# Performance work log

Hardware: AMD Instinct MI355X
Metric: run time of the kernel (lower is better)

## Reference

```python
import jax, jax.numpy as jnp
import numpy as np

B = 2; N_RAW = 16384; N_KP = 2048; M_VOX = 8192; C_VOX = 64
H_BEV, W_BEV, C_BEV, BEV_STRIDE = 200, 176, 256, 8
VOXEL_SIZE = np.array([0.05, 0.05, 0.1], np.float32)
PC_MIN = np.array([0.0, -40.0, -3.0], np.float32)
DOWNSAMPLE = 4
RAW_RADII = (0.4, 0.8); RAW_NS = (16, 16)
CONV_RADII = (1.2, 2.4); CONV_NS = (16, 32)
BN_SCALE = float(1.0 / np.sqrt(1.0 + 1e-5))  # eval-mode BN, running mean=0 var=1


def _fps_idx(pts, n):
    # farthest point sampling over pts [N,3] -> [n] int32 indices
    N = pts.shape[0]
    def step(carry, _):
        dists, last = carry
        d = jnp.sum((pts - pts[last]) ** 2, axis=-1)
        dists = jnp.minimum(dists, d)
        nxt = jnp.argmax(dists).astype(jnp.int32)
        return (dists, nxt), nxt
    init = (jnp.full((N,), 1e10, pts.dtype), jnp.int32(0))
    _, rest = jax.lax.scan(step, init, None, length=n - 1)
    return jnp.concatenate([jnp.zeros((1,), jnp.int32), rest])


def _bilinear(bev, x, y):
    # bev [H,W,C]; faithful to bilinear_interpolate_bev (clamp then weight)
    H, W, _ = bev.shape
    xf = jnp.floor(x); yf = jnp.floor(y)
    x0 = jnp.clip(xf.astype(jnp.int32), 0, W - 1)
    x1 = jnp.clip(xf.astype(jnp.int32) + 1, 0, W - 1)
    y0 = jnp.clip(yf.astype(jnp.int32), 0, H - 1)
    y1 = jnp.clip(yf.astype(jnp.int32) + 1, 0, H - 1)
    fa = bev[y1, x0]; fb = bev[y1, x1]; fc = bev[y0, x1]; fd = bev[y0, x0]
    x0f = x0.astype(x.dtype); x1f = x1.astype(x.dtype)
    y0f = y0.astype(y.dtype); y1f = y1.astype(y.dtype)
    wa = (x - x0f) * (y1f - y); wb = (x1f - x) * (y1f - y)
    wc = (x1f - x) * (y - y0f); wd = (x - x0f) * (y - y0f)
    return fd * wb[:, None] + fc * wa[:, None] + fa * wc[:, None] + fb * wd[:, None]


def _group(xyz, feats, new_xyz, radius, nsample):
    # ball query: first nsample points within radius (original order), pad with first hit
    M = xyz.shape[0]
    d2 = jnp.sum((new_xyz[:, None, :] - xyz[None, :, :]) ** 2, axis=-1)  # [K,M]
    mask = d2 < radius * radius
    key = jnp.where(mask, jnp.arange(M, dtype=jnp.int32)[None, :], M)
    idx = jnp.sort(key, axis=1)[:, :nsample]
    empty = ~jnp.any(mask, axis=1)
    idx = jnp.where(idx < M, idx, idx[:, :1])
    idx = jnp.clip(idx, 0, M - 1)
    g_xyz = xyz[idx] - new_xyz[:, None, :]
    g = jnp.concatenate([g_xyz, feats[idx]], axis=-1)  # [K,ns,3+C]
    return jnp.where(empty[:, None, None], 0.0, g), empty


def _bn_relu(x, g, b):
    return jax.nn.relu(x * (g * BN_SCALE) + b)


def _sa(xyz, feats, new_xyz, radii, nss, w0, g0, b0, w1, g1, b1):
    outs = []
    for i, (r, ns) in enumerate(zip(radii, nss)):
        grouped, empty = jax.vmap(lambda x, f, nx: _group(x, f, nx, r, ns))(xyz, feats, new_xyz)
        h = _bn_relu(grouped @ w0[i], g0[i], b0[i])
        h = _bn_relu(h @ w1[i], g1[i], b1[i])
        pooled = jnp.max(h, axis=2)  # [B,K,Cout]
        outs.append(jnp.where(empty[..., None], 0.0, pooled))
    return jnp.concatenate(outs, axis=-1)


def _forward(points, spatial_features, voxel_coords, voxel_features,
             raw_w0, raw_g0, raw_b0, raw_w1, raw_g1, raw_b1,
             conv_w0, conv_g0, conv_b0, conv_w1, conv_g1, conv_b1,
             fusion_w, fusion_g, fusion_b):
    pts = points.reshape(B, N_RAW, -1)
    xyz_raw = pts[..., 1:4]
    idxs = jax.vmap(lambda p: _fps_idx(p, N_KP))(jax.lax.stop_gradient(xyz_raw))
    kp = jnp.take_along_axis(xyz_raw, idxs[..., None], axis=1)  # [B,NKP,3]
    xi = (kp[..., 0] - PC_MIN[0]) / VOXEL_SIZE[0] / BEV_STRIDE
    yi = (kp[..., 1] - PC_MIN[1]) / VOXEL_SIZE[1] / BEV_STRIDE
    bev = jnp.transpose(spatial_features, (0, 2, 3, 1))  # [B,H,W,C]
    bev_feat = jax.vmap(_bilinear)(bev, xi, yi)  # [B,NKP,C_BEV]
    raw_feat = _sa(xyz_raw, pts[..., 4:], kp, RAW_RADII, RAW_NS,
                   raw_w0, raw_g0, raw_b0, raw_w1, raw_g1, raw_b1)
    vc = voxel_coords.reshape(B, M_VOX, 4)
    centers = (vc[..., jnp.array([3, 2, 1])].astype(jnp.float32) + 0.5) \
        * jnp.asarray(VOXEL_SIZE * DOWNSAMPLE) + jnp.asarray(PC_MIN)
    conv_feat = _sa(centers, voxel_features.reshape(B, M_VOX, C_VOX), kp, CONV_RADII, CONV_NS,
                    conv_w0, conv_g0, conv_b0, conv_w1, conv_g1, conv_b1)
    feats = jnp.concatenate([bev_feat, raw_feat, conv_feat], axis=-1).reshape(B * N_KP, -1)
    return _bn_relu(feats @ fusion_w, fusion_g, fusion_b)  # [B*NKP, 128]


def setup_inputs():
    key = jax.random.key(0)
    ks = jax.random.split(key, 8)
    xyz = jax.random.uniform(ks[0], (B * N_RAW, 3), jnp.float32) * jnp.array([70.4, 80.0, 4.0]) + jnp.array([0.0, -40.0, -3.0])
    inten = jax.random.uniform(ks[1], (B * N_RAW, 1), jnp.float32)
    bidx = jnp.repeat(jnp.arange(B, dtype=jnp.float32), N_RAW)[:, None]
    points = jnp.concatenate([bidx, xyz, inten], axis=1)
    spatial_features = jax.random.normal(ks[2], (B, C_BEV, H_BEV, W_BEV), jnp.float32)
    vb = jnp.repeat(jnp.arange(B, dtype=jnp.int32), M_VOX)[:, None]
    vz = jax.random.randint(ks[3], (B * M_VOX, 1), 0, 10, jnp.int32)
    vy = jax.random.randint(ks[4], (B * M_VOX, 1), 0, 400, jnp.int32)
    vx = jax.random.randint(ks[5], (B * M_VOX, 1), 0, 352, jnp.int32)
    voxel_coords = jnp.concatenate([vb, vz, vy, vx], axis=1)
    voxel_features = jax.random.normal(ks[6], (B * M_VOX, C_VOX), jnp.float32)
    pk = jax.random.split(ks[7], 5)
    w = lambda k, s: jax.random.normal(k, s, jnp.float32) * 0.05
    return dict(
        points=points, spatial_features=spatial_features,
        voxel_coords=voxel_coords, voxel_features=voxel_features,
        raw_w0=w(pk[0], (2, 4, 16)), raw_g0=jnp.ones((2, 16)), raw_b0=jnp.zeros((2, 16)),
        raw_w1=w(pk[1], (2, 16, 16)), raw_g1=jnp.ones((2, 16)), raw_b1=jnp.zeros((2, 16)),
        conv_w0=w(pk[2], (2, 67, 64)), conv_g0=jnp.ones((2, 64)), conv_b0=jnp.zeros((2, 64)),
        conv_w1=w(pk[3], (2, 64, 64)), conv_g1=jnp.ones((2, 64)), conv_b1=jnp.zeros((2, 64)),
        fusion_w=w(pk[4], (416, 128)), fusion_g=jnp.ones((128,)), fusion_b=jnp.zeros((128,)))


def reference(points, spatial_features, voxel_coords, voxel_features,
              raw_w0, raw_g0, raw_b0, raw_w1, raw_g1, raw_b1,
              conv_w0, conv_g0, conv_b0, conv_w1, conv_g1, conv_b1,
              fusion_w, fusion_g, fusion_b):
    return _forward(points, spatial_features, voxel_coords, voxel_features,
                    raw_w0, raw_g0, raw_b0, raw_w1, raw_g1, raw_b1,
                    conv_w0, conv_g0, conv_b0, conv_w1, conv_g1, conv_b1,
                    fusion_w, fusion_g, fusion_b)
```

## Files before the change

### kernel.cpp

```cpp
#include <hip/hip_runtime.h>


#define NRAW   16384
#define MVOX   8192
#define NKP    2048
#define NKPALL 4096

__device__ __constant__ float kBNS = (float)0.9999950000374997;

typedef float f32x2 __attribute__((ext_vector_type(2)));

__global__ __launch_bounds__(256) void prep_kernel(
    const float* __restrict__ pts, const int* __restrict__ vc,
    float4* __restrict__ xyz4, float4* __restrict__ cxyz4) {
#pragma clang fp contract(off)
  int i = blockIdx.x * 256 + threadIdx.x;
  if (i < 2 * NRAW) {
    const float* p = pts + (size_t)i * 5;
    xyz4[i] = make_float4(p[1], p[2], p[3], p[4]);
  }
  if (i < 2 * MVOX) {
    const int* v = vc + (size_t)i * 4;
    cxyz4[i] = make_float4(((float)v[3] + 0.5f) * 0.2f + 0.0f,
                           ((float)v[2] + 0.5f) * 0.2f + -40.0f,
                           ((float)v[1] + 0.5f) * 0.4f + -3.0f, 0.f);
  }
}

__global__ __launch_bounds__(1024) void sort_kernel(
    const float* __restrict__ pts, int* __restrict__ sperm) {
  const int b = blockIdx.x, t = threadIdx.x;
  __shared__ unsigned hist[256], cur[256];
  if (t < 256) hist[t] = 0u;
  __syncthreads();
  int bins[16];
#pragma unroll
  for (int k = 0; k < 16; ++k) {
    const int i = k * 1024 + t;
    const float y = pts[(size_t)(b * NRAW + i) * 5 + 2];
    int bin = (int)((y + 40.0f) * 3.2f);
    bin = bin < 0 ? 0 : (bin > 255 ? 255 : bin);
    bins[k] = bin;
    atomicAdd(&hist[bin], 1u);
  }
  __syncthreads();
  if (t == 0) {
    unsigned acc = 0;
    for (int i = 0; i < 256; ++i) { cur[i] = acc; acc += hist[i]; }
  }
  __syncthreads();
#pragma unroll
  for (int k = 0; k < 16; ++k) {
    const int i = k * 1024 + t;
    const unsigned pos = atomicAdd(&cur[bins[k]], 1u);
    sperm[b * NRAW + pos] = i;
  }
}

#define U64_STAGE(CTRL, RMASK)                                                 \
  {                                                                            \
    const unsigned tlo = (unsigned)__builtin_amdgcn_update_dpp(                \
        0, (int)lo, CTRL, RMASK, 0xf, true);                                   \
    const unsigned thi = (unsigned)__builtin_amdgcn_update_dpp(                \
        0, (int)hi, CTRL, RMASK, 0xf, true);                                   \
    const unsigned long long tv = ((unsigned long long)thi << 32) | tlo;       \
    const unsigned long long cv = ((unsigned long long)hi << 32) | lo;         \
    if (tv > cv) { hi = thi; lo = tlo; }                                       \
  }

__global__ __launch_bounds__(1024, 4) void fps_kernel(
    const int* __restrict__ sperm, const float4* __restrict__ xyz4,
    float* __restrict__ kx, float* __restrict__ ky, float* __restrict__ kz) {
#pragma clang fp contract(off)
  const int b = blockIdx.x;
  const int t = threadIdx.x;
  const int w = t >> 6, lane = t & 63;
  const int wb = w * 1024;
  const int base = b * NRAW;

  __shared__ unsigned long long slot[3];

  int pj[16];
  f32x2 px2[8], py2[8], pz2[8], dd2[8];
#pragma unroll
  for (int j = 0; j < 16; ++j)
    pj[j] = sperm[base + wb + j * 64 + lane];
#pragma unroll
  for (int j = 0; j < 16; ++j) {
    const float4 q = xyz4[base + pj[j]];
    px2[j >> 1][j & 1] = q.x;
    py2[j >> 1][j & 1] = q.y;
    pz2[j >> 1][j & 1] = q.z;
    dd2[j >> 1][j & 1] = 1e10f;
  }
  if (t < 3) slot[t] = 0ULL;

  float bnx = px2[0].x, bxx = px2[0].x, bny = py2[0].x, bxy = py2[0].x,
        bnz = pz2[0].x, bxz = pz2[0].x;
#pragma unroll
  for (int j = 1; j < 16; ++j) {
    bnx = fminf(bnx, px2[j >> 1][j & 1]); bxx = fmaxf(bxx, px2[j >> 1][j & 1]);
    bny = fminf(bny, py2[j >> 1][j & 1]); bxy = fmaxf(bxy, py2[j >> 1][j & 1]);
    bnz = fminf(bnz, pz2[j >> 1][j & 1]); bxz = fmaxf(bxz, pz2[j >> 1][j & 1]);
  }
#pragma unroll
  for (int off = 1; off < 64; off <<= 1) {
    bnx = fminf(bnx, __shfl_xor(bnx, off, 64));
    bxx = fmaxf(bxx, __shfl_xor(bxx, off, 64));
    bny = fminf(bny, __shfl_xor(bny, off, 64));
    bxy = fmaxf(bxy, __shfl_xor(bxy, off, 64));
    bnz = fminf(bnz, __shfl_xor(bnz, off, 64));
    bxz = fmaxf(bxz, __shfl_xor(bxz, off, 64));
  }

  const float4 p0 = xyz4[base];
  float lx = p0.x, ly = p0.y, lz = p0.z;
  if (t == 0) { kx[b * NKP] = lx; ky[b * NKP] = ly; kz[b * NKP] = lz; }

  unsigned long long cpk = 0ULL;
  float bvc = __builtin_inff();
  __syncthreads();

  for (int s = 1; s < NKP; ++s) {
    float dxm = fmaxf(fmaxf(bnx - lx, lx - bxx), 0.f);
    float dym = fmaxf(fmaxf(bny - ly, ly - bxy), 0.f);
    float dzm = fmaxf(fmaxf(bnz - lz, lz - bxz), 0.f);
    const float LB2 = dxm * dxm + dym * dym + dzm * dzm;
    if (!(LB2 * 0.9999f > bvc)) {
      const f32x2 lx2 = {lx, lx}, ly2 = {ly, ly}, lz2 = {lz, lz};
#pragma unroll
      for (int j8 = 0; j8 < 8; ++j8) {
        f32x2 dx = px2[j8] - lx2;
        f32x2 dy = py2[j8] - ly2;
        f32x2 dz = pz2[j8] - lz2;
        f32x2 d2 = dx * dx;
        d2 = d2 + dy * dy;
        d2 = d2 + dz * dz;
        dd2[j8] = __builtin_elementwise_min(dd2[j8], d2);
      }
      f32x2 t0 = __builtin_elementwise_max(dd2[0], dd2[1]);
      f32x2 t1 = __builtin_elementwise_max(dd2[2], dd2[3]);
      f32x2 t2 = __builtin_elementwise_max(dd2[4], dd2[5]);
      f32x2 t3 = __builtin_elementwise_max(dd2[6], dd2[7]);
      t0 = __builtin_elementwise_max(t0, t1);
      t2 = __builtin_elementwise_max(t2, t3);
      t0 = __builtin_elementwise_max(t0, t2);
      const float bv = fmaxf(t0.x, t0.y);
      const unsigned vb = __float_as_uint(bv);
      unsigned mo = 0xFFFFFFFFu;
#pragma unroll
      for (int j = 0; j < 16; ++j)
        if (__float_as_uint(dd2[j >> 1][j & 1]) == vb) {
          const unsigned o = (unsigned)pj[j];
          mo = o < mo ? o : mo;
        }
      unsigned hi = vb, lo = ~mo;
      U64_STAGE(0xB1,  0xf)
      U64_STAGE(0x4E,  0xf)
      U64_STAGE(0x124, 0xf)
      U64_STAGE(0x128, 0xf)
      U64_STAGE(0x142, 0xa)
      U64_STAGE(0x143, 0xc)
      bvc = __uint_as_float(
          (unsigned)__builtin_amdgcn_readlane((int)hi, 63));
      cpk = ((unsigned long long)hi << 32) | (unsigned long long)lo;
    }
    if (lane == 63) atomicMax(&slot[s % 3], cpk);
    __syncthreads();

    const unsigned long long g = slot[s % 3];
    const int wi = __builtin_amdgcn_readfirstlane((int)~(unsigned)g);
    if (t == 0) slot[(s + 2) % 3] = 0ULL;
    const float4 cw = xyz4[base + wi];
    lx = cw.x; ly = cw.y; lz = cw.z;
    if (t == 0) { kx[b * NKP + s] = lx; ky[b * NKP + s] = ly; kz[b * NKP + s] = lz; }
  }
}

__global__ __launch_bounds__(256) void bev_kernel(
    const float* __restrict__ sf, const float* __restrict__ kx,
    const float* __restrict__ ky, float* __restrict__ feats) {
#pragma clang fp contract(off)
  const int kidx = blockIdx.x;
  const int c = threadIdx.x;
  const int b = kidx >> 11;
  const float x = (kx[kidx] - 0.0f) / 0.05f / 8.0f;
  const float y = (ky[kidx] - (-40.0f)) / 0.05f / 8.0f;
  const float xf = floorf(x), yf = floorf(y);
  int x0 = (int)xf;     x0 = x0 < 0 ? 0 : (x0 > 175 ? 175 : x0);
  int x1 = (int)xf + 1; x1 = x1 < 0 ? 0 : (x1 > 175 ? 175 : x1);
  int y0 = (int)yf;     y0 = y0 < 0 ? 0 : (y0 > 199 ? 199 : y0);
  int y1 = (int)yf + 1; y1 = y1 < 0 ? 0 : (y1 > 199 ? 199 : y1);
  const float x0f = (float)x0, x1f = (float)x1, y0f = (float)y0, y1f = (float)y1;
  const float wa = (x - x0f) * (y1f - y);
  const float wb = (x1f - x) * (y1f - y);
  const float wc = (x1f - x) * (y - y0f);
  const float wd = (x - x0f) * (y - y0f);
  const float* base = sf + ((size_t)b * 256 + c) * (200 * 176);
  const float fa = base[y1 * 176 + x0];
  const float fb = base[y1 * 176 + x1];
  const float fc = base[y0 * 176 + x1];
  const float fd = base[y0 * 176 + x0];
  float r = fd * wb; r = r + fc * wa; r = r + fa * wc; r = r + fb * wd;
  feats[(size_t)kidx * 416 + c] = r;
}

__global__ __launch_bounds__(256) void raw_sa_kernel(
    const float4* __restrict__ xyz4,
    const float* __restrict__ kx, const float* __restrict__ ky,
    const float* __restrict__ kz,
    const float* __restrict__ w0, const float* __restrict__ g0,
    const float* __restrict__ b0, const float* __restrict__ w1,
    const float* __restrict__ g1, const float* __restrict__ b1,
    float* __restrict__ feats) {
  const int wv = threadIdx.x >> 6;
  const int lane = threadIdx.x & 63;
  const int gw = blockIdx.x * 4 + wv;
  const int ri = gw >> 12;
  const int kidx = gw & 4095;
  const int b = kidx >> 11;
  const float R2 = ri ? (float)(0.8 * 0.8) : (float)(0.4 * 0.4);

  __shared__ int   idxl[4][16];
  __shared__ float hbuf[4][16][17];

  const float kxv = kx[kidx], kyv = ky[kidx], kzv = kz[kidx];
  const int base = b * NRAW;
  int cnt = 0;
  {
#pragma clang fp contract(off)
    for (int ch = 0; ch < NRAW / 64 && cnt < 16; ++ch) {
      const float4 q = xyz4[base + ch * 64 + lane];
      float dx = kxv - q.x, dy = kyv - q.y, dz = kzv - q.z;
      float d2 = dx * dx; d2 = d2 + dy * dy; d2 = d2 + dz * dz;
      unsigned long long m = __ballot(d2 < R2);
      while (m && cnt < 16) {
        int bit = __builtin_ctzll(m);
        if (lane == 0) idxl[wv][cnt] = ch * 64 + bit;
        ++cnt;
        m &= m - 1;
      }
    }
  }
  const int outoff = kidx * 416 + 256 + ri * 16;
  if (cnt == 0) {
    if (lane < 16) feats[outoff + lane] = 0.f;
    return;
  }
  __threadfence_block();

  const int s = lane & 15, cq = lane >> 4;
  const int ss = (s < cnt) ? s : 0;
  const float4 q = xyz4[base + idxl[wv][ss]];
  const float gx = q.x - kxv, gy = q.y - kyv, gz = q.z - kzv, gi = q.w;
  const int wb0 = ri * 64, cb = ri * 16;
#pragma unroll
  for (int j = 0; j < 4; ++j) {
    int c = cq * 4 + j;
    float a = gx * w0[wb0 + c];
    a = fmaf(gy, w0[wb0 + 16 + c], a);
    a = fmaf(gz, w0[wb0 + 32 + c], a);
    a = fmaf(gi, w0[wb0 + 48 + c], a);
    a = fmaf(a, g0[cb + c] * kBNS, b0[cb + c]);
    hbuf[wv][s][c] = fmaxf(a, 0.f);
  }
  __threadfence_block();
  float o0 = 0.f, o1 = 0.f, o2 = 0.f, o3 = 0.f;
  const int wb1 = ri * 256;
#pragma unroll
  for (int k = 0; k < 16; ++k) {
    float hk = hbuf[wv][s][k];
    o0 = fmaf(hk, w1[wb1 + k * 16 + cq * 4 + 0], o0);
    o1 = fmaf(hk, w1[wb1 + k * 16 + cq * 4 + 1], o1);
    o2 = fmaf(hk, w1[wb1 + k * 16 + cq * 4 + 2], o2);
    o3 = fmaf(hk, w1[wb1 + k * 16 + cq * 4 + 3], o3);
  }
  float v0 = fmaxf(fmaf(o0, g1[cb + cq * 4 + 0] * kBNS, b1[cb + cq * 4 + 0]), 0.f);
  float v1 = fmaxf(fmaf(o1, g1[cb + cq * 4 + 1] * kBNS, b1[cb + cq * 4 + 1]), 0.f);
  float v2 = fmaxf(fmaf(o2, g1[cb + cq * 4 + 2] * kBNS, b1[cb + cq * 4 + 2]), 0.f);
  float v3 = fmaxf(fmaf(o3, g1[cb + cq * 4 + 3] * kBNS, b1[cb + cq * 4 + 3]), 0.f);
#pragma unroll
  for (int off = 1; off < 16; off <<= 1) {
    v0 = fmaxf(v0, __shfl_xor(v0, off, 64));
    v1 = fmaxf(v1, __shfl_xor(v1, off, 64));
    v2 = fmaxf(v2, __shfl_xor(v2, off, 64));
    v3 = fmaxf(v3, __shfl_xor(v3, off, 64));
  }
  if (s == 0) {
    feats[outoff + cq * 4 + 0] = v0;
    feats[outoff + cq * 4 + 1] = v1;
    feats[outoff + cq * 4 + 2] = v2;
    feats[outoff + cq * 4 + 3] = v3;
  }
}

__global__ __launch_bounds__(256) void conv_sa_kernel(
    const float4* __restrict__ cxyz4, const float* __restrict__ vf,
    const float* __restrict__ kx, const float* __restrict__ ky,
    const float* __restrict__ kz,
    const float* __restrict__ w0, const float* __restrict__ g0,
    const float* __restrict__ b0, const float* __restrict__ w1,
    const float* __restrict__ g1, const float* __restrict__ b1,
    float* __restrict__ feats) {
  const int wv = threadIdx.x >> 6;
  const int lane = threadIdx.x & 63;
  const int gw = blockIdx.x * 4 + wv;
  const int ri = gw >> 12;
  const int kidx = gw & 4095;
  const int b = kidx >> 11;
  const int NS = ri ? 32 : 16;
  const float R2 = ri ? (float)(2.4 * 2.4) : (float)(1.2 * 1.2);

  __shared__ int   idxl[4][32];
  __shared__ float gbuf[4][64];
  __shared__ float hbuf[4][32][64];

  const float kxv = kx[kidx], kyv = ky[kidx], kzv = kz[kidx];
  const int base = b * MVOX;
  int cnt = 0;
  {
#pragma clang fp contract(off)
    for (int ch = 0; ch < MVOX / 64 && cnt < NS; ++ch) {
      const float4 q = cxyz4[base + ch * 64 + lane];
      float dx = kxv - q.x, dy = kyv - q.y, dz = kzv - q.z;
      float d2 = dx * dx; d2 = d2 + dy * dy; d2 = d2 + dz * dz;
      unsigned long long m = __ballot(d2 < R2);
      while (m && cnt < NS) {
        int bit = __builtin_ctzll(m);
        if (lane == 0) idxl[wv][cnt] = ch * 64 + bit;
        ++cnt;
        m &= m - 1;
      }
    }
  }
  const int outoff = kidx * 416 + 288 + ri * 64;
  if (cnt == 0) {
    feats[outoff + lane] = 0.f;
    return;
  }
  __threadfence_block();

  const float wA0 = w0[(ri * 67 + 0) * 64 + lane];
  const float wA1 = w0[(ri * 67 + 1) * 64 + lane];
  const float wA2 = w0[(ri * 67 + 2) * 64 + lane];
  float wB[64];
#pragma unroll
  for (int k = 0; k < 64; ++k) wB[k] = w0[(ri * 67 + 3 + k) * 64 + lane];
  float wC[64];
#pragma unroll
  for (int k = 0; k < 64; ++k) wC[k] = w1[(ri * 64 + k) * 64 + lane];
  const float s0 = g0[ri * 64 + lane] * kBNS, bb0 = b0[ri * 64 + lane];
  const float s1 = g1[ri * 64 + lane] * kBNS, bb1 = b1[ri * 64 + lane];

  for (int sm = 0; sm < cnt; ++sm) {
    const int p = base + idxl[wv][sm];
    const float4 q = cxyz4[p];
    const float ox = q.x - kxv, oy = q.y - kyv, oz = q.z - kzv;
    gbuf[wv][lane] = vf[(size_t)p * 64 + lane];
    __threadfence_block();
    float acc = ox * wA0;
    acc = fmaf(oy, wA1, acc);
    acc = fmaf(oz, wA2, acc);
#pragma unroll
    for (int k4 = 0; k4 < 16; ++k4) {
      float4 g4 = *(const float4*)&gbuf[wv][k4 * 4];
      acc = fmaf(g4.x, wB[k4 * 4 + 0], acc);
      acc = fmaf(g4.y, wB[k4 * 4 + 1], acc);
      acc = fmaf(g4.z, wB[k4 * 4 + 2], acc);
      acc = fmaf(g4.w, wB[k4 * 4 + 3], acc);
    }
    hbuf[wv][sm][lane] = fmaxf(fmaf(acc, s0, bb0), 0.f);
    __threadfence_block();
  }
  float mx = -1e30f;
  for (int sm = 0; sm < cnt; ++sm) {
    float acc = 0.f;
#pragma unroll
    for (int k4 = 0; k4 < 16; ++k4) {
      float4 h4 = *(const float4*)&hbuf[wv][sm][k4 * 4];
      acc = fmaf(h4.x, wC[k4 * 4 + 0], acc);
      acc = fmaf(h4.y, wC[k4 * 4 + 1], acc);
      acc = fmaf(h4.z, wC[k4 * 4 + 2], acc);
      acc = fmaf(h4.w, wC[k4 * 4 + 3], acc);
    }
    mx = fmaxf(mx, fmaxf(fmaf(acc, s1, bb1), 0.f));
  }
  feats[outoff + lane] = mx;
}

__global__ __launch_bounds__(256) void fusion_kernel(
    const float* __restrict__ feats, const float* __restrict__ fw,
    const float* __restrict__ fg, const float* __restrict__ fb,
    float* __restrict__ out) {
  const int gid = blockIdx.x * 256 + threadIdx.x;
  const int kidx = gid >> 7, c = gid & 127;
  const float* f = feats + (size_t)kidx * 416;
  float acc = 0.f;
#pragma unroll 4
  for (int k = 0; k < 416; k += 4) {
    float4 fv = *(const float4*)(f + k);
    acc = fmaf(fv.x, fw[(k + 0) * 128 + c], acc);
    acc = fmaf(fv.y, fw[(k + 1) * 128 + c], acc);
    acc = fmaf(fv.z, fw[(k + 2) * 128 + c], acc);
    acc = fmaf(fv.w, fw[(k + 3) * 128 + c], acc);
  }
  out[gid] = fmaxf(fmaf(acc, fg[c] * kBNS, fb[c]), 0.f);
}

extern "C" void kernel_launch(void* const* d_in, const int* in_sizes, int n_in,
                              void* d_out, int out_size, void* d_ws, size_t ws_size,
                              hipStream_t stream) {
  (void)in_sizes; (void)n_in; (void)out_size; (void)ws_size;
  const float* pts = (const float*)d_in[0];
  const float* sf  = (const float*)d_in[1];
  const int*   vc  = (const int*)d_in[2];
  const float* vf  = (const float*)d_in[3];
  const float* raw_w0 = (const float*)d_in[4];
  const float* raw_g0 = (const float*)d_in[5];
  const float* raw_b0 = (const float*)d_in[6];
  const float* raw_w1 = (const float*)d_in[7];
  const float* raw_g1 = (const float*)d_in[8];
  const float* raw_b1 = (const float*)d_in[9];
  const float* conv_w0 = (const float*)d_in[10];
  const float* conv_g0 = (const float*)d_in[11];
  const float* conv_b0 = (const float*)d_in[12];
  const float* conv_w1 = (const float*)d_in[13];
  const float* conv_g1 = (const float*)d_in[14];
  const float* conv_b1 = (const float*)d_in[15];
  const float* fus_w = (const float*)d_in[16];
  const float* fus_g = (const float*)d_in[17];
  const float* fus_b = (const float*)d_in[18];
  float* out = (float*)d_out;

  float* W = (float*)d_ws;
  float4* xyz4  = (float4*)W;
  float4* cxyz4 = (float4*)(W + 131072);
  float* kx    = W + 196608;
  float* ky    = W + 200704;
  float* kz    = W + 204800;
  float* feats = W + 208896;
  int* sperm = (int*)(W + 208896);

  prep_kernel<<<128, 256, 0, stream>>>(pts, vc, xyz4, cxyz4);
  sort_kernel<<<2, 1024, 0, stream>>>(pts, sperm);
  fps_kernel<<<2, 1024, 0, stream>>>(sperm, xyz4, kx, ky, kz);
  bev_kernel<<<NKPALL, 256, 0, stream>>>(sf, kx, ky, feats);
  raw_sa_kernel<<<2048, 256, 0, stream>>>(xyz4, kx, ky, kz,
                                          raw_w0, raw_g0, raw_b0, raw_w1, raw_g1, raw_b1,
                                          feats);
  conv_sa_kernel<<<2048, 256, 0, stream>>>(cxyz4, vf, kx, ky, kz,
                                           conv_w0, conv_g0, conv_b0, conv_w1, conv_g1, conv_b1,
                                           feats);
  fusion_kernel<<<2048, 256, 0, stream>>>(feats, fus_w, fus_g, fus_b, out);
}
```

Measured before the change: 2.198 ms.

## Fuse FPS with downstream stages via persistent workers polling progress flags

Merges the FPS, BEV sampling, raw and voxel set-abstraction and fusion kernels into one persistent launch. Two blocks run FPS and publish a release-ordered progress counter every 16 keypoints, while 224 worker blocks spin on that counter and process each keypoint as soon as it exists. Per-keypoint features stay in LDS instead of a global buffer, and conv weights are staged in LDS rather than per-lane registers. This hides the downstream work behind the serial FPS loop, at the cost of relying on all blocks being co-resident (risk of deadlock otherwise), spin-wait overhead, and workers competing with the FPS blocks for CU resources.

New measurement: 3.135 ms. 42.6% more time.

```diff
diff --git a/kernel.cpp b/kernel.cpp
--- a/kernel.cpp
+++ b/kernel.cpp
@@ -1,10 +1,12 @@
 #include <hip/hip_runtime.h>
 
 
-#define NRAW   16384
-#define MVOX   8192
-#define NKP    2048
-#define NKPALL 4096
+#define NRAW    16384
+#define MVOX    8192
+#define NKP     2048
+#define NKPALL  4096
+#define NWORKER 224
+#define NBLK    (NWORKER + 2)
 
 __device__ __constant__ float kBNS = (float)0.9999950000374997;
 
@@ -68,343 +70,337 @@
     if (tv > cv) { hi = thi; lo = tlo; }                                       \
   }
 
-__global__ __launch_bounds__(1024, 4) void fps_kernel(
+__global__ __launch_bounds__(1024, 1) void fused_kernel(
     const int* __restrict__ sperm, const float4* __restrict__ xyz4,
-    float* __restrict__ kx, float* __restrict__ ky, float* __restrict__ kz) {
+    const float4* __restrict__ cxyz4, const float* __restrict__ vf,
+    const float* __restrict__ sf,
+    const float* __restrict__ rw0, const float* __restrict__ rg0,
+    const float* __restrict__ rb0, const float* __restrict__ rw1,
+    const float* __restrict__ rg1, const float* __restrict__ rb1,
+    const float* __restrict__ cw0, const float* __restrict__ cg0,
+    const float* __restrict__ cb0, const float* __restrict__ cw1,
+    const float* __restrict__ cg1, const float* __restrict__ cb1,
+    const float* __restrict__ fw, const float* __restrict__ fg,
+    const float* __restrict__ fb,
+    float* __restrict__ kx, float* __restrict__ ky, float* __restrict__ kz,
+    int* prog, float* __restrict__ out) {
+  const int t = threadIdx.x;
+  const int wv = t >> 6, lane = t & 63;
+
+  __shared__ unsigned long long slot[3];
+  __shared__ float ldsW0[2 * 67 * 64];
+  __shared__ float ldsW1[2 * 64 * 64];
+  __shared__ int   idxlC[2][32];
+  __shared__ __align__(16) float gbuf[2][64];
+  __shared__ __align__(16) float hbufC[2][32][64];
+  __shared__ int   idxlR[2][16];
+  __shared__ float hbufR[2][16][17];
+  __shared__ __align__(16) float featsL[416];
+  __shared__ float kxyz[4];
+
+  if (blockIdx.x < 2) {
 #pragma clang fp contract(off)
-  const int b = blockIdx.x;
-  const int t = threadIdx.x;
-  const int w = t >> 6, lane = t & 63;
-  const int wb = w * 1024;
-  const int base = b * NRAW;
-
-  __shared__ unsigned long long slot[3];
-
-  int pj[16];
-  f32x2 px2[8], py2[8], pz2[8], dd2[8];
-#pragma unroll
-  for (int j = 0; j < 16; ++j)
-    pj[j] = sperm[base + wb + j * 64 + lane];
-#pragma unroll
-  for (int j = 0; j < 16; ++j) {
-    const float4 q = xyz4[base + pj[j]];
-    px2[j >> 1][j & 1] = q.x;
-    py2[j >> 1][j & 1] = q.y;
-    pz2[j >> 1][j & 1] = q.z;
-    dd2[j >> 1][j & 1] = 1e10f;
-  }
-  if (t < 3) slot[t] = 0ULL;
-
-  float bnx = px2[0].x, bxx = px2[0].x, bny = py2[0].x, bxy = py2[0].x,
-        bnz = pz2[0].x, bxz = pz2[0].x;
-#pragma unroll
-  for (int j = 1; j < 16; ++j) {
-    bnx = fminf(bnx, px2[j >> 1][j & 1]); bxx = fmaxf(bxx, px2[j >> 1][j & 1]);
-    bny = fminf(bny, py2[j >> 1][j & 1]); bxy = fmaxf(bxy, py2[j >> 1][j & 1]);
-    bnz = fminf(bnz, pz2[j >> 1][j & 1]); bxz = fmaxf(bxz, pz2[j >> 1][j & 1]);
-  }
-#pragma unroll
-  for (int off = 1; off < 64; off <<= 1) {
-    bnx = fminf(bnx, __shfl_xor(bnx, off, 64));
-    bxx = fmaxf(bxx, __shfl_xor(bxx, off, 64));
-    bny = fminf(bny, __shfl_xor(bny, off, 64));
-    bxy = fmaxf(bxy, __shfl_xor(bxy, off, 64));
-    bnz = fminf(bnz, __shfl_xor(bnz, off, 64));
-    bxz = fmaxf(bxz, __shfl_xor(bxz, off, 64));
-  }
-
-  const float4 p0 = xyz4[base];
-  float lx = p0.x, ly = p0.y, lz = p0.z;
-  if (t == 0) { kx[b * NKP] = lx; ky[b * NKP] = ly; kz[b * NKP] = lz; }
-
-  unsigned long long cpk = 0ULL;
-  float bvc = __builtin_inff();
-  __syncthreads();
-
-  for (int s = 1; s < NKP; ++s) {
-    float dxm = fmaxf(fmaxf(bnx - lx, lx - bxx), 0.f);
-    float dym = fmaxf(fmaxf(bny - ly, ly - bxy), 0.f);
-    float dzm = fmaxf(fmaxf(bnz - lz, lz - bxz), 0.f);
-    const float LB2 = dxm * dxm + dym * dym + dzm * dzm;
-    if (!(LB2 * 0.9999f > bvc)) {
-      const f32x2 lx2 = {lx, lx}, ly2 = {ly, ly}, lz2 = {lz, lz};
-#pragma unroll
-      for (int j8 = 0; j8 < 8; ++j8) {
-        f32x2 dx = px2[j8] - lx2;
-        f32x2 dy = py2[j8] - ly2;
-        f32x2 dz = pz2[j8] - lz2;
-        f32x2 d2 = dx * dx;
-        d2 = d2 + dy * dy;
-        d2 = d2 + dz * dz;
-        dd2[j8] = __builtin_elementwise_min(dd2[j8], d2);
+    const int b = blockIdx.x;
+    const int wb = wv * 1024;
+    const int base = b * NRAW;
+
+    int pj[16];
+    f32x2 px2[8], py2[8], pz2[8], dd2[8];
+#pragma unroll
+    for (int j = 0; j < 16; ++j)
+      pj[j] = sperm[base + wb + j * 64 + lane];
+#pragma unroll
+    for (int j = 0; j < 16; ++j) {
+      const float4 q = xyz4[base + pj[j]];
+      px2[j >> 1][j & 1] = q.x;
+      py2[j >> 1][j & 1] = q.y;
+      pz2[j >> 1][j & 1] = q.z;
+      dd2[j >> 1][j & 1] = 1e10f;
+    }
+    if (t < 3) slot[t] = 0ULL;
+
+    float bnx = px2[0].x, bxx = px2[0].x, bny = py2[0].x, bxy = py2[0].x,
+          bnz = pz2[0].x, bxz = pz2[0].x;
+#pragma unroll
+    for (int j = 1; j < 16; ++j) {
+      bnx = fminf(bnx, px2[j >> 1][j & 1]); bxx = fmaxf(bxx, px2[j >> 1][j & 1]);
+      bny = fminf(bny, py2[j >> 1][j & 1]); bxy = fmaxf(bxy, py2[j >> 1][j & 1]);
+      bnz = fminf(bnz, pz2[j >> 1][j & 1]); bxz = fmaxf(bxz, pz2[j >> 1][j & 1]);
+    }
+#pragma unroll
+    for (int off = 1; off < 64; off <<= 1) {
+      bnx = fminf(bnx, __shfl_xor(bnx, off, 64));
+      bxx = fmaxf(bxx, __shfl_xor(bxx, off, 64));
+      bny = fminf(bny, __shfl_xor(bny, off, 64));
+      bxy = fmaxf(bxy, __shfl_xor(bxy, off, 64));
+      bnz = fminf(bnz, __shfl_xor(bnz, off, 64));
+      bxz = fmaxf(bxz, __shfl_xor(bxz, off, 64));
+    }
+
+    const float4 p0 = xyz4[base];
+    float lx = p0.x, ly = p0.y, lz = p0.z;
+    if (t == 0) { kx[b * NKP] = lx; ky[b * NKP] = ly; kz[b * NKP] = lz; }
+
+    unsigned long long cpk = 0ULL;
+    float bvc = __builtin_inff();
+    __syncthreads();
+
+    for (int s = 1; s < NKP; ++s) {
+      float dxm = fmaxf(fmaxf(bnx - lx, lx - bxx), 0.f);
+      float dym = fmaxf(fmaxf(bny - ly, ly - bxy), 0.f);
+      float dzm = fmaxf(fmaxf(bnz - lz, lz - bxz), 0.f);
+      const float LB2 = dxm * dxm + dym * dym + dzm * dzm;
+      if (!(LB2 * 0.9999f > bvc)) {
+        const f32x2 lx2 = {lx, lx}, ly2 = {ly, ly}, lz2 = {lz, lz};
+#pragma unroll
+        for (int j8 = 0; j8 < 8; ++j8) {
+          f32x2 dx = px2[j8] - lx2;
+          f32x2 dy = py2[j8] - ly2;
+          f32x2 dz = pz2[j8] - lz2;
+          f32x2 d2 = dx * dx;
+          d2 = d2 + dy * dy;
+          d2 = d2 + dz * dz;
+          dd2[j8] = __builtin_elementwise_min(dd2[j8], d2);
+        }
+        f32x2 t0 = __builtin_elementwise_max(dd2[0], dd2[1]);
+        f32x2 t1 = __builtin_elementwise_max(dd2[2], dd2[3]);
+        f32x2 t2 = __builtin_elementwise_max(dd2[4], dd2[5]);
+        f32x2 t3 = __builtin_elementwise_max(dd2[6], dd2[7]);
+        t0 = __builtin_elementwise_max(t0, t1);
+        t2 = __builtin_elementwise_max(t2, t3);
+        t0 = __builtin_elementwise_max(t0, t2);
+        const float bv = fmaxf(t0.x, t0.y);
+        const unsigned vb = __float_as_uint(bv);
+        unsigned mo = 0xFFFFFFFFu;
+#pragma unroll
+        for (int j = 0; j < 16; ++j)
+          if (__float_as_uint(dd2[j >> 1][j & 1]) == vb) {
+            const unsigned o = (unsigned)pj[j];
+            mo = o < mo ? o : mo;
+          }
+        unsigned hi = vb, lo = ~mo;
+        U64_STAGE(0xB1,  0xf)
+        U64_STAGE(0x4E,  0xf)
+        U64_STAGE(0x124, 0xf)
+        U64_STAGE(0x128, 0xf)
+        U64_STAGE(0x142, 0xa)
+        U64_STAGE(0x143, 0xc)
+        bvc = __uint_as_float(
+            (unsigned)__builtin_amdgcn_readlane((int)hi, 63));
+        cpk = ((unsigned long long)hi << 32) | (unsigned long long)lo;
       }
-      f32x2 t0 = __builtin_elementwise_max(dd2[0], dd2[1]);
-      f32x2 t1 = __builtin_elementwise_max(dd2[2], dd2[3]);
-      f32x2 t2 = __builtin_elementwise_max(dd2[4], dd2[5]);
-      f32x2 t3 = __builtin_elementwise_max(dd2[6], dd2[7]);
-      t0 = __builtin_elementwise_max(t0, t1);
-      t2 = __builtin_elementwise_max(t2, t3);
-      t0 = __builtin_elementwise_max(t0, t2);
-      const float bv = fmaxf(t0.x, t0.y);
-      const unsigned vb = __float_as_uint(bv);
-      unsigned mo = 0xFFFFFFFFu;
-#pragma unroll
-      for (int j = 0; j < 16; ++j)
-        if (__float_as_uint(dd2[j >> 1][j & 1]) == vb) {
-          const unsigned o = (unsigned)pj[j];
-          mo = o < mo ? o : mo;
-        }
-      unsigned hi = vb, lo = ~mo;
-      U64_STAGE(0xB1,  0xf)
-      U64_STAGE(0x4E,  0xf)
-      U64_STAGE(0x124, 0xf)
-      U64_STAGE(0x128, 0xf)
-      U64_STAGE(0x142, 0xa)
-      U64_STAGE(0x143, 0xc)
-      bvc = __uint_as_float(
-          (unsigned)__builtin_amdgcn_readlane((int)hi, 63));
-      cpk = ((unsigned long long)hi << 32) | (unsigned long long)lo;
-    }
-    if (lane == 63) atomicMax(&slot[s % 3], cpk);
-    __syncthreads();
-
-    const unsigned long long g = slot[s % 3];
-    const int wi = __builtin_amdgcn_readfirstlane((int)~(unsigned)g);
-    if (t == 0) slot[(s + 2) % 3] = 0ULL;
-    const float4 cw = xyz4[base + wi];
-    lx = cw.x; ly = cw.y; lz = cw.z;
-    if (t == 0) { kx[b * NKP + s] = lx; ky[b * NKP + s] = ly; kz[b * NKP + s] = lz; }
-  }
-}
-
-__global__ __launch_bounds__(256) void bev_kernel(
-    const float* __restrict__ sf, const float* __restrict__ kx,
-    const float* __restrict__ ky, float* __restrict__ feats) {
-#pragma clang fp contract(off)
-  const int kidx = blockIdx.x;
-  const int c = threadIdx.x;
-  const int b = kidx >> 11;
-  const float x = (kx[kidx] - 0.0f) / 0.05f / 8.0f;
-  const float y = (ky[kidx] - (-40.0f)) / 0.05f / 8.0f;
-  const float xf = floorf(x), yf = floorf(y);
-  int x0 = (int)xf;     x0 = x0 < 0 ? 0 : (x0 > 175 ? 175 : x0);
-  int x1 = (int)xf + 1; x1 = x1 < 0 ? 0 : (x1 > 175 ? 175 : x1);
-  int y0 = (int)yf;     y0 = y0 < 0 ? 0 : (y0 > 199 ? 199 : y0);
-  int y1 = (int)yf + 1; y1 = y1 < 0 ? 0 : (y1 > 199 ? 199 : y1);
-  const float x0f = (float)x0, x1f = (float)x1, y0f = (float)y0, y1f = (float)y1;
-  const float wa = (x - x0f) * (y1f - y);
-  const float wb = (x1f - x) * (y1f - y);
-  const float wc = (x1f - x) * (y - y0f);
-  const float wd = (x - x0f) * (y - y0f);
-  const float* base = sf + ((size_t)b * 256 + c) * (200 * 176);
-  const float fa = base[y1 * 176 + x0];
-  const float fb = base[y1 * 176 + x1];
-  const float fc = base[y0 * 176 + x1];
-  const float fd = base[y0 * 176 + x0];
-  float r = fd * wb; r = r + fc * wa; r = r + fa * wc; r = r + fb * wd;
-  feats[(size_t)kidx * 416 + c] = r;
-}
-
-__global__ __launch_bounds__(256) void raw_sa_kernel(
-    const float4* __restrict__ xyz4,
-    const float* __restrict__ kx, const float* __restrict__ ky,
-    const float* __restrict__ kz,
-    const float* __restrict__ w0, const float* __restrict__ g0,
-    const float* __restrict__ b0, const float* __restrict__ w1,
-    const float* __restrict__ g1, const float* __restrict__ b1,
-    float* __restrict__ feats) {
-  const int wv = threadIdx.x >> 6;
-  const int lane = threadIdx.x & 63;
-  const int gw = blockIdx.x * 4 + wv;
-  const int ri = gw >> 12;
-  const int kidx = gw & 4095;
-  const int b = kidx >> 11;
-  const float R2 = ri ? (float)(0.8 * 0.8) : (float)(0.4 * 0.4);
-
-  __shared__ int   idxl[4][16];
-  __shared__ float hbuf[4][16][17];
-
-  const float kxv = kx[kidx], kyv = ky[kidx], kzv = kz[kidx];
-  const int base = b * NRAW;
-  int cnt = 0;
-  {
-#pragma clang fp contract(off)
-    for (int ch = 0; ch < NRAW / 64 && cnt < 16; ++ch) {
-      const float4 q = xyz4[base + ch * 64 + lane];
-      float dx = kxv - q.x, dy = kyv - q.y, dz = kzv - q.z;
-      float d2 = dx * dx; d2 = d2 + dy * dy; d2 = d2 + dz * dz;
-      unsigned long long m = __ballot(d2 < R2);
-      while (m && cnt < 16) {
-        int bit = __builtin_ctzll(m);
-        if (lane == 0) idxl[wv][cnt] = ch * 64 + bit;
-        ++cnt;
-        m &= m - 1;
+      if (lane == 63) atomicMax(&slot[s % 3], cpk);
+      __syncthreads();
+
+      const unsigned long long g = slot[s % 3];
+      const int wi = __builtin_amdgcn_readfirstlane((int)~(unsigned)g);
+      if (t == 0) slot[(s + 2) % 3] = 0ULL;
+      const float4 cw = xyz4[base + wi];
+      lx = cw.x; ly = cw.y; lz = cw.z;
+      if (t == 0) {
+        kx[b * NKP + s] = lx; ky[b * NKP + s] = ly; kz[b * NKP + s] = lz;
+        if ((s & 15) == 15)
+          __hip_atomic_store(&prog[b], s + 1, __ATOMIC_RELEASE,
+                             __HIP_MEMORY_SCOPE_AGENT);
       }
     }
-  }
-  const int outoff = kidx * 416 + 256 + ri * 16;
-  if (cnt == 0) {
-    if (lane < 16) feats[outoff + lane] = 0.f;
-    return;
-  }
-  __threadfence_block();
-
-  const int s = lane & 15, cq = lane >> 4;
-  const int ss = (s < cnt) ? s : 0;
-  const float4 q = xyz4[base + idxl[wv][ss]];
-  const float gx = q.x - kxv, gy = q.y - kyv, gz = q.z - kzv, gi = q.w;
-  const int wb0 = ri * 64, cb = ri * 16;
-#pragma unroll
-  for (int j = 0; j < 4; ++j) {
-    int c = cq * 4 + j;
-    float a = gx * w0[wb0 + c];
-    a = fmaf(gy, w0[wb0 + 16 + c], a);
-    a = fmaf(gz, w0[wb0 + 32 + c], a);
-    a = fmaf(gi, w0[wb0 + 48 + c], a);
-    a = fmaf(a, g0[cb + c] * kBNS, b0[cb + c]);
-    hbuf[wv][s][c] = fmaxf(a, 0.f);
-  }
-  __threadfence_block();
-  float o0 = 0.f, o1 = 0.f, o2 = 0.f, o3 = 0.f;
-  const int wb1 = ri * 256;
-#pragma unroll
-  for (int k = 0; k < 16; ++k) {
-    float hk = hbuf[wv][s][k];
-    o0 = fmaf(hk, w1[wb1 + k * 16 + cq * 4 + 0], o0);
-    o1 = fmaf(hk, w1[wb1 + k * 16 + cq * 4 + 1], o1);
-    o2 = fmaf(hk, w1[wb1 + k * 16 + cq * 4 + 2], o2);
-    o3 = fmaf(hk, w1[wb1 + k * 16 + cq * 4 + 3], o3);
-  }
-  float v0 = fmaxf(fmaf(o0, g1[cb + cq * 4 + 0] * kBNS, b1[cb + cq * 4 + 0]), 0.f);
-  float v1 = fmaxf(fmaf(o1, g1[cb + cq * 4 + 1] * kBNS, b1[cb + cq * 4 + 1]), 0.f);
-  float v2 = fmaxf(fmaf(o2, g1[cb + cq * 4 + 2] * kBNS, b1[cb + cq * 4 + 2]), 0.f);
-  float v3 = fmaxf(fmaf(o3, g1[cb + cq * 4 + 3] * kBNS, b1[cb + cq * 4 + 3]), 0.f);
-#pragma unroll
-  for (int off = 1; off < 16; off <<= 1) {
-    v0 = fmaxf(v0, __shfl_xor(v0, off, 64));
-    v1 = fmaxf(v1, __shfl_xor(v1, off, 64));
-    v2 = fmaxf(v2, __shfl_xor(v2, off, 64));
-    v3 = fmaxf(v3, __shfl_xor(v3, off, 64));
-  }
-  if (s == 0) {
-    feats[outoff + cq * 4 + 0] = v0;
-    feats[outoff + cq * 4 + 1] = v1;
-    feats[outoff + cq * 4 + 2] = v2;
-    feats[outoff + cq * 4 + 3] = v3;
-  }
-}
-
-__global__ __launch_bounds__(256) void conv_sa_kernel(
-    const float4* __restrict__ cxyz4, const float* __restrict__ vf,
-    const float* __restrict__ kx, const float* __restrict__ ky,
-    const float* __restrict__ kz,
-    const float* __restrict__ w0, const float* __restrict__ g0,
-    const float* __restrict__ b0, const float* __restrict__ w1,
-    const float* __restrict__ g1, const float* __restrict__ b1,
-    float* __restrict__ feats) {
-  const int wv = threadIdx.x >> 6;
-  const int lane = threadIdx.x & 63;
-  const int gw = blockIdx.x * 4 + wv;
-  const int ri = gw >> 12;
-  const int kidx = gw & 4095;
-  const int b = kidx >> 11;
-  const int NS = ri ? 32 : 16;
-  const float R2 = ri ? (float)(2.4 * 2.4) : (float)(1.2 * 1.2);
-
-  __shared__ int   idxl[4][32];
-  __shared__ float gbuf[4][64];
-  __shared__ float hbuf[4][32][64];
-
-  const float kxv = kx[kidx], kyv = ky[kidx], kzv = kz[kidx];
-  const int base = b * MVOX;
-  int cnt = 0;
-  {
+  } else {
+    for (int i = t; i < 2 * 67 * 64; i += 1024) ldsW0[i] = cw0[i];
+    for (int i = t; i < 2 * 64 * 64; i += 1024) ldsW1[i] = cw1[i];
+    __syncthreads();
+
+    const int wkr = (int)blockIdx.x - 2;
+    for (int g = wkr; g < NKPALL; g += NWORKER) {
+      const int bb = g >> 11, s = g & 2047;
+      const int kidx = g;
+      if (t == 0) {
+        while (__hip_atomic_load(&prog[bb], __ATOMIC_ACQUIRE,
+                                 __HIP_MEMORY_SCOPE_AGENT) <= s)
+          __builtin_amdgcn_s_sleep(8);
+        kxyz[0] = kx[kidx]; kxyz[1] = ky[kidx]; kxyz[2] = kz[kidx];
+      }
+      __syncthreads();
+      const float kxv = kxyz[0], kyv = kxyz[1], kzv = kxyz[2];
+
+      if (wv < 2) {
+        const int ri = wv;
+        const float R2 = ri ? (float)(0.8 * 0.8) : (float)(0.4 * 0.4);
+        const int rbase = bb * NRAW;
+        int cnt = 0;
+        {
 #pragma clang fp contract(off)
-    for (int ch = 0; ch < MVOX / 64 && cnt < NS; ++ch) {
-      const float4 q = cxyz4[base + ch * 64 + lane];
-      float dx = kxv - q.x, dy = kyv - q.y, dz = kzv - q.z;
-      float d2 = dx * dx; d2 = d2 + dy * dy; d2 = d2 + dz * dz;
-      unsigned long long m = __ballot(d2 < R2);
-      while (m && cnt < NS) {
-        int bit = __builtin_ctzll(m);
-        if (lane == 0) idxl[wv][cnt] = ch * 64 + bit;
-        ++cnt;
-        m &= m - 1;
+          for (int ch = 0; ch < NRAW / 64 && cnt < 16; ++ch) {
+            const float4 q = xyz4[rbase + ch * 64 + lane];
+            float dx = kxv - q.x, dy = kyv - q.y, dz = kzv - q.z;
+            float d2 = dx * dx; d2 = d2 + dy * dy; d2 = d2 + dz * dz;
+            unsigned long long m = __ballot(d2 < R2);
+            while (m && cnt < 16) {
+              int bit = __builtin_ctzll(m);
+              if (lane == 0) idxlR[ri][cnt] = ch * 64 + bit;
+              ++cnt;
+              m &= m - 1;
+            }
+          }
+        }
+        const int outoff = 256 + ri * 16;
+        if (cnt == 0) {
+          if (lane < 16) featsL[outoff + lane] = 0.f;
+        } else {
+          __threadfence_block();
+          const int sL = lane & 15, cq = lane >> 4;
+          const int ss = (sL < cnt) ? sL : 0;
+          const float4 q = xyz4[rbase + idxlR[ri][ss]];
+          const float gx = q.x - kxv, gy = q.y - kyv, gz = q.z - kzv, gi = q.w;
+          const int wb0 = ri * 64, cb = ri * 16;
+#pragma unroll
+          for (int j = 0; j < 4; ++j) {
+            int c = cq * 4 + j;
+            float a = gx * rw0[wb0 + c];
+            a = fmaf(gy, rw0[wb0 + 16 + c], a);
+            a = fmaf(gz, rw0[wb0 + 32 + c], a);
+            a = fmaf(gi, rw0[wb0 + 48 + c], a);
+            a = fmaf(a, rg0[cb + c] * kBNS, rb0[cb + c]);
+            hbufR[ri][sL][c] = fmaxf(a, 0.f);
+          }
+          __threadfence_block();
+          float o0 = 0.f, o1 = 0.f, o2 = 0.f, o3 = 0.f;
+          const int wb1 = ri * 256;
+#pragma unroll
+          for (int k = 0; k < 16; ++k) {
+            float hk = hbufR[ri][sL][k];
+            o0 = fmaf(hk, rw1[wb1 + k * 16 + cq * 4 + 0], o0);
+            o1 = fmaf(hk, rw1[wb1 + k * 16 + cq * 4 + 1], o1);
+            o2 = fmaf(hk, rw1[wb1 + k * 16 + cq * 4 + 2], o2);
+            o3 = fmaf(hk, rw1[wb1 + k * 16 + cq * 4 + 3], o3);
+          }
+          float v0 = fmaxf(fmaf(o0, rg1[cb + cq * 4 + 0] * kBNS, rb1[cb + cq * 4 + 0]), 0.f);
+          float v1 = fmaxf(fmaf(o1, rg1[cb + cq * 4 + 1] * kBNS, rb1[cb + cq * 4 + 1]), 0.f);
+          float v2 = fmaxf(fmaf(o2, rg1[cb + cq * 4 + 2] * kBNS, rb1[cb + cq * 4 + 2]), 0.f);
+          float v3 = fmaxf(fmaf(o3, rg1[cb + cq * 4 + 3] * kBNS, rb1[cb + cq * 4 + 3]), 0.f);
+#pragma unroll
+          for (int off = 1; off < 16; off <<= 1) {
+            v0 = fmaxf(v0, __shfl_xor(v0, off, 64));
+            v1 = fmaxf(v1, __shfl_xor(v1, off, 64));
+            v2 = fmaxf(v2, __shfl_xor(v2, off, 64));
+            v3 = fmaxf(v3, __shfl_xor(v3, off, 64));
+          }
+          if (sL == 0) {
+            featsL[outoff + cq * 4 + 0] = v0;
+            featsL[outoff + cq * 4 + 1] = v1;
+            featsL[outoff + cq * 4 + 2] = v2;
+            featsL[outoff + cq * 4 + 3] = v3;
+          }
+        }
+      } else if (wv < 4) {
+        const int ri = wv - 2;
+        const int NS = ri ? 32 : 16;
+        const float R2 = ri ? (float)(2.4 * 2.4) : (float)(1.2 * 1.2);
+        const int cbase = bb * MVOX;
+        int cnt = 0;
+        {
+#pragma clang fp contract(off)
+          for (int ch = 0; ch < MVOX / 64 && cnt < NS; ++ch) {
+            const float4 q = cxyz4[cbase + ch * 64 + lane];
+            float dx = kxv - q.x, dy = kyv - q.y, dz = kzv - q.z;
+            float d2 = dx * dx; d2 = d2 + dy * dy; d2 = d2 + dz * dz;
+            unsigned long long m = __ballot(d2 < R2);
+            while (m && cnt < NS) {
+              int bit = __builtin_ctzll(m);
+              if (lane == 0) idxlC[ri][cnt] = ch * 64 + bit;
+              ++cnt;
+              m &= m - 1;
+            }
+          }
+        }
+        const int outoff = 288 + ri * 64;
+        if (cnt == 0) {
+          featsL[outoff + lane] = 0.f;
+        } else {
+          __threadfence_block();
+          const float wA0 = ldsW0[(ri * 67 + 0) * 64 + lane];
+          const float wA1 = ldsW0[(ri * 67 + 1) * 64 + lane];
+          const float wA2 = ldsW0[(ri * 67 + 2) * 64 + lane];
+          const float* wB = &ldsW0[(ri * 67 + 3) * 64 + lane];
+          const float* wC = &ldsW1[ri * 64 * 64 + lane];
+          const float s0 = cg0[ri * 64 + lane] * kBNS, bb0 = cb0[ri * 64 + lane];
+          const float s1 = cg1[ri * 64 + lane] * kBNS, bb1 = cb1[ri * 64 + lane];
+          for (int sm = 0; sm < cnt; ++sm) {
+            const int p = cbase + idxlC[ri][sm];
+            const float4 q = cxyz4[p];
+            const float ox = q.x - kxv, oy = q.y - kyv, oz = q.z - kzv;
+            gbuf[ri][lane] = vf[(size_t)p * 64 + lane];
+            __threadfence_block();
+            float acc = ox * wA0;
+            acc = fmaf(oy, wA1, acc);
+            acc = fmaf(oz, wA2, acc);
+#pragma unroll
+            for (int k4 = 0; k4 < 16; ++k4) {
+              float4 g4 = *(const float4*)&gbuf[ri][k4 * 4];
+              acc = fmaf(g4.x, wB[(k4 * 4 + 0) * 64], acc);
+              acc = fmaf(g4.y, wB[(k4 * 4 + 1) * 64], acc);
+              acc = fmaf(g4.z, wB[(k4 * 4 + 2) * 64], acc);
+              acc = fmaf(g4.w, wB[(k4 * 4 + 3) * 64], acc);
+            }
+            hbufC[ri][sm][lane] = fmaxf(fmaf(acc, s0, bb0), 0.f);
+            __threadfence_block();
+          }
+          float mx = -1e30f;
+          for (int sm = 0; sm < cnt; ++sm) {
+            float acc = 0.f;
+#pragma unroll
+            for (int k4 = 0; k4 < 16; ++k4) {
+              float4 h4 = *(const float4*)&hbufC[ri][sm][k4 * 4];
+              acc = fmaf(h4.x, wC[(k4 * 4 + 0) * 64], acc);
+              acc = fmaf(h4.y, wC[(k4 * 4 + 1) * 64], acc);
+              acc = fmaf(h4.z, wC[(k4 * 4 + 2) * 64], acc);
+              acc = fmaf(h4.w, wC[(k4 * 4 + 3) * 64], acc);
+            }
+            mx = fmaxf(mx, fmaxf(fmaf(acc, s1, bb1), 0.f));
+          }
+          featsL[outoff + lane] = mx;
+        }
+      } else if (wv < 8) {
+#pragma clang fp contract(off)
+        const int c = t - 256;
+        const float x = (kxv - 0.0f) / 0.05f / 8.0f;
+        const float y = (kyv - (-40.0f)) / 0.05f / 8.0f;
+        const float xf = floorf(x), yf = floorf(y);
+        int x0 = (int)xf;     x0 = x0 < 0 ? 0 : (x0 > 175 ? 175 : x0);
+        int x1 = (int)xf + 1; x1 = x1 < 0 ? 0 : (x1 > 175 ? 175 : x1);
+        int y0 = (int)yf;     y0 = y0 < 0 ? 0 : (y0 > 199 ? 199 : y0);
+        int y1 = (int)yf + 1; y1 = y1 < 0 ? 0 : (y1 > 199 ? 199 : y1);
+        const float x0f = (float)x0, x1f = (float)x1, y0f = (float)y0, y1f = (float)y1;
+        const float wa = (x - x0f) * (y1f - y);
+        const float wbv = (x1f - x) * (y1f - y);
+        const float wc = (x1f - x) * (y - y0f);
+        const float wd = (x - x0f) * (y - y0f);
+        const float* bsf = sf + ((size_t)bb * 256 + c) * (200 * 176);
+        const float fa = bsf[y1 * 176 + x0];
+        const float fbv = bsf[y1 * 176 + x1];
+        const float fc = bsf[y0 * 176 + x1];
+        const float fd = bsf[y0 * 176 + x0];
+        float r = fd * wbv; r = r + fc * wa; r = r + fa * wc; r = r + fbv * wd;
+        featsL[c] = r;
       }
+      __syncthreads();
+
+      if (t < 128) {
+        const int c = t;
+        float acc = 0.f;
+#pragma unroll 4
+        for (int k = 0; k < 416; k += 4) {
+          float4 fv = *(const float4*)(featsL + k);
+          acc = fmaf(fv.x, fw[(k + 0) * 128 + c], acc);
+          acc = fmaf(fv.y, fw[(k + 1) * 128 + c], acc);
+          acc = fmaf(fv.z, fw[(k + 2) * 128 + c], acc);
+          acc = fmaf(fv.w, fw[(k + 3) * 128 + c], acc);
+        }
+        out[(size_t)kidx * 128 + c] =
+            fmaxf(fmaf(acc, fg[c] * kBNS, fb[c]), 0.f);
+      }
+      __syncthreads();
     }
   }
-  const int outoff = kidx * 416 + 288 + ri * 64;
-  if (cnt == 0) {
-    feats[outoff + lane] = 0.f;
-    return;
-  }
-  __threadfence_block();
-
-  const float wA0 = w0[(ri * 67 + 0) * 64 + lane];
-  const float wA1 = w0[(ri * 67 + 1) * 64 + lane];
-  const float wA2 = w0[(ri * 67 + 2) * 64 + lane];
-  float wB[64];
-#pragma unroll
-  for (int k = 0; k < 64; ++k) wB[k] = w0[(ri * 67 + 3 + k) * 64 + lane];
-  float wC[64];
-#pragma unroll
-  for (int k = 0; k < 64; ++k) wC[k] = w1[(ri * 64 + k) * 64 + lane];
-  const float s0 = g0[ri * 64 + lane] * kBNS, bb0 = b0[ri * 64 + lane];
-  const float s1 = g1[ri * 64 + lane] * kBNS, bb1 = b1[ri * 64 + lane];
-
-  for (int sm = 0; sm < cnt; ++sm) {
-    const int p = base + idxl[wv][sm];
-    const float4 q = cxyz4[p];
-    const float ox = q.x - kxv, oy = q.y - kyv, oz = q.z - kzv;
-    gbuf[wv][lane] = vf[(size_t)p * 64 + lane];
-    __threadfence_block();
-    float acc = ox * wA0;
-    acc = fmaf(oy, wA1, acc);
-    acc = fmaf(oz, wA2, acc);
-#pragma unroll
-    for (int k4 = 0; k4 < 16; ++k4) {
-      float4 g4 = *(const float4*)&gbuf[wv][k4 * 4];
-      acc = fmaf(g4.x, wB[k4 * 4 + 0], acc);
-      acc = fmaf(g4.y, wB[k4 * 4 + 1], acc);
-      acc = fmaf(g4.z, wB[k4 * 4 + 2], acc);
-      acc = fmaf(g4.w, wB[k4 * 4 + 3], acc);
-    }
-    hbuf[wv][sm][lane] = fmaxf(fmaf(acc, s0, bb0), 0.f);
-    __threadfence_block();
-  }
-  float mx = -1e30f;
-  for (int sm = 0; sm < cnt; ++sm) {
-    float acc = 0.f;
-#pragma unroll
-    for (int k4 = 0; k4 < 16; ++k4) {
-      float4 h4 = *(const float4*)&hbuf[wv][sm][k4 * 4];
-      acc = fmaf(h4.x, wC[k4 * 4 + 0], acc);
-      acc = fmaf(h4.y, wC[k4 * 4 + 1], acc);
-      acc = fmaf(h4.z, wC[k4 * 4 + 2], acc);
-      acc = fmaf(h4.w, wC[k4 * 4 + 3], acc);
-    }
-    mx = fmaxf(mx, fmaxf(fmaf(acc, s1, bb1), 0.f));
-  }
-  feats[outoff + lane] = mx;
-}
-
-__global__ __launch_bounds__(256) void fusion_kernel(
-    const float* __restrict__ feats, const float* __restrict__ fw,
-    const float* __restrict__ fg, const float* __restrict__ fb,
-    float* __restrict__ out) {
-  const int gid = blockIdx.x * 256 + threadIdx.x;
-  const int kidx = gid >> 7, c = gid & 127;
-  const float* f = feats + (size_t)kidx * 416;
-  float acc = 0.f;
-#pragma unroll 4
-  for (int k = 0; k < 416; k += 4) {
-    float4 fv = *(const float4*)(f + k);
-    acc = fmaf(fv.x, fw[(k + 0) * 128 + c], acc);
-    acc = fmaf(fv.y, fw[(k + 1) * 128 + c], acc);
-    acc = fmaf(fv.z, fw[(k + 2) * 128 + c], acc);
-    acc = fmaf(fv.w, fw[(k + 3) * 128 + c], acc);
-  }
-  out[gid] = fmaxf(fmaf(acc, fg[c] * kBNS, fb[c]), 0.f);
 }
 
 extern "C" void kernel_launch(void* const* d_in, const int* in_sizes, int n_in,
@@ -438,18 +434,15 @@
   float* kx    = W + 196608;
   float* ky    = W + 200704;
   float* kz    = W + 204800;
-  float* feats = W + 208896;
-  int* sperm = (int*)(W + 208896);
-
+  int*   prog  = (int*)(W + 208896);
+  int*   sperm = (int*)(W + 209920);
+
+  hipMemsetAsync(prog, 0, 2 * sizeof(int), stream);
   prep_kernel<<<128, 256, 0, stream>>>(pts, vc, xyz4, cxyz4);
   sort_kernel<<<2, 1024, 0, stream>>>(pts, sperm);
-  fps_kernel<<<2, 1024, 0, stream>>>(sperm, xyz4, kx, ky, kz);
-  bev_kernel<<<NKPALL, 256, 0, stream>>>(sf, kx, ky, feats);
-  raw_sa_kernel<<<2048, 256, 0, stream>>>(xyz4, kx, ky, kz,
-                                          raw_w0, raw_g0, raw_b0, raw_w1, raw_g1, raw_b1,
-                                          feats);
-  conv_sa_kernel<<<2048, 256, 0, stream>>>(cxyz4, vf, kx, ky, kz,
-                                           conv_w0, conv_g0, conv_b0, conv_w1, conv_g1, conv_b1,
-                                           feats);
-  fusion_kernel<<<2048, 256, 0, stream>>>(feats, fus_w, fus_g, fus_b, out);
+  fused_kernel<<<NBLK, 1024, 0, stream>>>(
+      sperm, xyz4, cxyz4, vf, sf,
+      raw_w0, raw_g0, raw_b0, raw_w1, raw_g1, raw_b1,
+      conv_w0, conv_g0, conv_b0, conv_w1, conv_g1, conv_b1,
+      fus_w, fus_g, fus_b, kx, ky, kz, prog, out);
 }
```
